# Kernel tuning notes

Measured on AMD Instinct MI355X. Metric: run time of the kernel, lower is better.

## Reference

```python
import jax, jax.numpy as jnp
import numpy as np

B, N, INP = 16, 1024, 256
HEADS, DIM_HEAD = 8, 32
INNER = HEADS * DIM_HEAD  # 256
OUP = 256
IH = IW = 32  # IH*IW == N


def _relative_index(ih, iw):
    # mirrors the torch __init__ construction (meshgrid indexing='ij')
    coords = np.stack(np.meshgrid(np.arange(ih), np.arange(iw), indexing='ij')).reshape(2, -1)
    rel = coords[:, :, None] - coords[:, None, :]  # [2, N, N]
    rel[0] += ih - 1
    rel[1] += iw - 1
    rel[0] *= 2 * iw - 1
    return rel.sum(0).reshape(-1)  # [N*N]


def setup_inputs() -> dict:
    key = jax.random.key(0)
    kx, kqkv, kout, kbias = jax.random.split(key, 4)
    x = jax.random.normal(kx, (B, N, INP), dtype=jnp.float32)
    w_qkv = jax.random.normal(kqkv, (INP, 3 * INNER), dtype=jnp.float32) * 0.02
    w_out = jax.random.normal(kout, (INNER, OUP), dtype=jnp.float32) * 0.02
    b_out = jnp.zeros((OUP,), dtype=jnp.float32)
    bias_table = jax.random.normal(kbias, ((2 * IH - 1) * (2 * IW - 1), HEADS), dtype=jnp.float32) * 0.02
    relative_index = jnp.asarray(_relative_index(IH, IW), dtype=jnp.int32)
    return {"x": x, "w_qkv": w_qkv, "w_out": w_out, "b_out": b_out,
            "bias_table": bias_table, "relative_index": relative_index}


def reference(x, w_qkv, w_out, b_out, bias_table, relative_index):
    b, n, _ = x.shape
    scale = DIM_HEAD ** (-0.5)
    qkv = x @ w_qkv  # [b, n, 3*inner]
    q, k, v = jnp.split(qkv, 3, axis=-1)
    split_heads = lambda t: t.reshape(b, n, HEADS, DIM_HEAD).transpose(0, 2, 1, 3)  # b h n d
    q, k, v = split_heads(q), split_heads(k), split_heads(v)
    dots = jnp.einsum('bhnd,bhmd->bhnm', q, k) * scale  # [b, h, n, n]
    # gather bias: (n*n, heads) -> (1, heads, n, n), matching '(h w) c -> 1 c h w'
    rel_bias = bias_table[relative_index].reshape(n, n, HEADS).transpose(2, 0, 1)[None]
    attn = jax.nn.softmax(dots + rel_bias, axis=-1)
    out = jnp.einsum('bhnm,bhmd->bhnd', attn, v)
    out = out.transpose(0, 2, 1, 3).reshape(b, n, INNER)  # b n (h d)
    return out @ w_out + b_out
```

## Files before the change

kernel.cpp:

```cpp
#include <hip/hip_runtime.h>
#include <hip/hip_bf16.h>

typedef __bf16 bf16;
typedef bf16 bf16x4 __attribute__((ext_vector_type(4)));
typedef bf16 bf16x8 __attribute__((ext_vector_type(8)));
typedef short s16x4 __attribute__((ext_vector_type(4)));
typedef float f32x4 __attribute__((ext_vector_type(4)));

#define MFMA32(A, B, C) __builtin_amdgcn_mfma_f32_16x16x32_bf16(A, B, C, 0, 0, 0)
#define MFMA16(A, B, C) __builtin_amdgcn_mfma_f32_16x16x16bf16_1k(A, B, C, 0, 0, 0)
#define GL2LDS16(gp, lp)                                                            \
  __builtin_amdgcn_global_load_lds((const __attribute__((address_space(1))) unsigned int*)(gp), \
                                   (__attribute__((address_space(3))) unsigned int*)(lp), 16, 0, 0)

static constexpr float SCALE = 0.17677669529663687f;
static constexpr float LOG2E = 1.4426950408889634f;

__global__ __launch_bounds__(256) void k_prep(const float* __restrict__ x,
                                              const float* __restrict__ wqkv,
                                              const float* __restrict__ wout,
                                              const float* __restrict__ table,
                                              const int* __restrict__ ridx,
                                              bf16* __restrict__ xb, bf16* __restrict__ wtq,
                                              bf16* __restrict__ wto, bf16* __restrict__ rbb) {
  const int tid = threadIdx.x;
  const int blk = blockIdx.x;
  if (blk < 2048) {
    int t = blk * 256 + tid;
    const float4* s = reinterpret_cast<const float4*>(x) + (size_t)t * 2;
    float4 a = s[0], c = s[1];
    bf16x8 o;
    o[0] = (bf16)a.x; o[1] = (bf16)a.y; o[2] = (bf16)a.z; o[3] = (bf16)a.w;
    o[4] = (bf16)c.x; o[5] = (bf16)c.y; o[6] = (bf16)c.z; o[7] = (bf16)c.w;
    reinterpret_cast<bf16x8*>(xb)[t] = o;
  } else if (blk < 3072) {
    int t = (blk - 2048) * 256 + tid;
    if (t < 196608) {
      int n = t >> 8, k = t & 255;
      wtq[t] = (bf16)wqkv[k * 768 + n];
    } else {
      int t2 = t - 196608;
      int n = t2 >> 8, k = t2 & 255;
      wto[t2] = (bf16)wout[k * 256 + n];
    }
  } else {
    const int bb2 = blk - 3072;
    const int qt = bb2 >> 6, kt = bb2 & 63;
    const int r = tid & 3, lane = tid >> 2;
    const int ln = lane & 15, quad = lane >> 4;
    const int qrow = qt * 16 + ln;
    const int key = kt * 16 + quad * 4 + r;
    const int idx = ridx[qrow * 1024 + key];
    const float4* p = reinterpret_cast<const float4*>(table) + idx * 2;
    float4 a = p[0], c = p[1];
    float vals[8] = {a.x, a.y, a.z, a.w, c.x, c.y, c.z, c.w};
    const int base = bb2 * 256 + tid;
#pragma unroll
    for (int h = 0; h < 8; ++h) rbb[h * 1048576 + base] = (bf16)(vals[h] * LOG2E);
  }
}

template <int EPI>
__global__ __launch_bounds__(256) void k_gemm(const bf16* __restrict__ A,
                                              const bf16* __restrict__ Bt,
                                              bf16* __restrict__ q, bf16* __restrict__ kk,
                                              bf16* __restrict__ vt, float* __restrict__ out,
                                              const float* __restrict__ bout) {
  __shared__ __align__(16) bf16 As[2][4096];
  __shared__ __align__(16) bf16 Bs[2][4096];
  const int tid = threadIdx.x;
  const int ln = tid & 15, quad = (tid >> 4) & 3, wv = tid >> 6;
  const int wm = (wv >> 1) * 64, wn = (wv & 1) * 64;
  const int m0 = blockIdx.x * 128, n0 = blockIdx.y * 128;
  const int srow = tid >> 2, scg = (tid & 3) * 8;
  const bf16* ag = A + (size_t)(m0 + srow) * 256 + scg;
  const bf16* bg = Bt + (size_t)(n0 + srow) * 256 + scg;
  f32x4 acc[4][4] = {};

  GL2LDS16(ag, &As[0][tid * 8]);
  GL2LDS16(ag + 64 * 256, &As[0][2048 + tid * 8]);
  GL2LDS16(bg, &Bs[0][tid * 8]);
  GL2LDS16(bg + 64 * 256, &Bs[0][2048 + tid * 8]);

#pragma unroll 2
  for (int kt = 0; kt < 256; kt += 32) {
    const int cur = (kt >> 5) & 1, nxt = cur ^ 1;
    __syncthreads();
    if (kt < 224) {
      GL2LDS16(ag + kt + 32, &As[nxt][tid * 8]);
      GL2LDS16(ag + 64 * 256 + kt + 32, &As[nxt][2048 + tid * 8]);
      GL2LDS16(bg + kt + 32, &Bs[nxt][tid * 8]);
      GL2LDS16(bg + 64 * 256 + kt + 32, &Bs[nxt][2048 + tid * 8]);
    }
    bf16x8 af[4], bfr[4];
#pragma unroll
    for (int i = 0; i < 4; ++i)
      af[i] = *reinterpret_cast<const bf16x8*>(&As[cur][(wm + i * 16 + ln) * 32 + quad * 8]);
#pragma unroll
    for (int i = 0; i < 4; ++i)
      bfr[i] = *reinterpret_cast<const bf16x8*>(&Bs[cur][(wn + i * 16 + ln) * 32 + quad * 8]);
#pragma unroll
    for (int i = 0; i < 4; ++i)
#pragma unroll
      for (int j = 0; j < 4; ++j) acc[i][j] = MFMA32(af[i], bfr[j], acc[i][j]);
  }

  if (EPI == 0) {
    const int colbase = n0 + wn;
    const int seg = colbase >> 8;
    const int cb = colbase & 255;
    const float mul = (seg == 0) ? SCALE * LOG2E : 1.0f;
#pragma unroll
    for (int i = 0; i < 4; ++i) {
      const int gm = m0 + wm + i * 16 + quad * 4;
      const int b = gm >> 10;
#pragma unroll
      for (int j = 0; j < 4; ++j) {
        const int gc = cb + j * 16 + ln;
        const int h = gc >> 5, d = gc & 31;
#pragma unroll
        for (int r = 0; r < 4; ++r) {
          const int nseq = (gm + r) & 1023;
          if (seg == 2) {
            vt[(b * 8 + h) * 32768 + d * 1024 + nseq] = (bf16)acc[i][j][r];
          } else {
            bf16* dst = (seg == 0) ? q : kk;
            dst[(b * 8 + h) * 32768 + nseq * 32 + d] = (bf16)(acc[i][j][r] * mul);
          }
        }
      }
    }
  } else {
#pragma unroll
    for (int j = 0; j < 4; ++j) {
      const int gc = n0 + wn + j * 16 + ln;
      const float bb = bout[gc];
#pragma unroll
      for (int i = 0; i < 4; ++i) {
        const int gm = m0 + wm + i * 16 + quad * 4;
#pragma unroll
        for (int r = 0; r < 4; ++r) out[(size_t)(gm + r) * 256 + gc] = acc[i][j][r] + bb;
      }
    }
  }
}

__global__ __launch_bounds__(256, 4) void k_flash(const bf16* __restrict__ qs,
                                                  const bf16* __restrict__ ks,
                                                  const bf16* __restrict__ vtg,
                                                  const bf16* __restrict__ rbb,
                                                  bf16* __restrict__ ao) {
  __shared__ __align__(16) bf16 Ks[2][2048];
  __shared__ __align__(16) bf16 Vs[2][2048];
  const int tid = threadIdx.x;
  const int lane = tid & 63;
  const int ln = lane & 15, quad = lane >> 4, wv = tid >> 6;
  const int blk = blockIdx.x;
  const int bh = blk & 127;
  const int b = bh >> 3, h = bh & 7;
  const int qtw = (blk >> 7) * 4 + wv;
  const int q0 = qtw * 32;
  const bf16* qb = qs + bh * 32768;
  const bf16* kb = ks + bh * 32768;
  const bf16* vb = vtg + bh * 32768;
  const bf16* bbias0 = rbb + h * 1048576 + (2 * qtw) * 16384 + lane * 4;
  const bf16* bbias1 = bbias0 + 16384;

  const bf16* kg = kb + (tid >> 2) * 32 + (((tid & 3) ^ ((tid >> 3) & 3)) * 8);
  const bf16* vg = vb + (tid >> 3) * 1024 + (((tid & 7) ^ ((tid >> 3) & 7)) * 8);

  const bf16x8 qfrag0 = *reinterpret_cast<const bf16x8*>(&qb[(q0 + ln) * 32 + quad * 8]);
  const bf16x8 qfrag1 = *reinterpret_cast<const bf16x8*>(&qb[(q0 + 16 + ln) * 32 + quad * 8]);

  const int ksw = (quad ^ ((ln >> 1) & 3)) * 8;
  const int vswl = ln & 7;

  f32x4 a00 = {0.f, 0.f, 0.f, 0.f}, a01 = {0.f, 0.f, 0.f, 0.f};
  f32x4 a10 = {0.f, 0.f, 0.f, 0.f}, a11 = {0.f, 0.f, 0.f, 0.f};
  float lsum0 = 0.f, lsum1 = 0.f;

  bf16x4 cbf[2][2][4];
#pragma unroll
  for (int nt = 0; nt < 4; ++nt) {
    cbf[0][0][nt] = *reinterpret_cast<const bf16x4*>(&bbias0[nt * 256]);
    cbf[0][1][nt] = *reinterpret_cast<const bf16x4*>(&bbias1[nt * 256]);
  }
  GL2LDS16(kg, &Ks[0][tid * 8]);
  GL2LDS16(vg, &Vs[0][tid * 8]);

#pragma unroll 2
  for (int it = 0; it < 16; ++it) {
    const int cur = it & 1, nxt = cur ^ 1;
    const int k0 = it * 64;
    __syncthreads();
    if (it < 15) {
      GL2LDS16(kg + (k0 + 64) * 32, &Ks[nxt][tid * 8]);
      GL2LDS16(vg + k0 + 64, &Vs[nxt][tid * 8]);
#pragma unroll
      for (int nt = 0; nt < 4; ++nt) {
        cbf[nxt][0][nt] = *reinterpret_cast<const bf16x4*>(&bbias0[((it + 1) * 4 + nt) * 256]);
        cbf[nxt][1][nt] = *reinterpret_cast<const bf16x4*>(&bbias1[((it + 1) * 4 + nt) * 256]);
      }
    }
    bf16x8 kf[4];
#pragma unroll
    for (int nt = 0; nt < 4; ++nt)
      kf[nt] = *reinterpret_cast<const bf16x8*>(&Ks[cur][(nt * 16 + ln) * 32 + ksw]);
    s16x4 vfa[4], vfc[4];
#pragma unroll
    for (int nt = 0; nt < 4; ++nt) {
      const int col = ((2 * nt + (quad >> 1)) ^ vswl) * 8 + (quad & 1) * 4;
      vfa[nt] = *reinterpret_cast<const s16x4*>(&Vs[cur][ln * 64 + col]);
      vfc[nt] = *reinterpret_cast<const s16x4*>(&Vs[cur][(ln + 16) * 64 + col]);
    }
    f32x4 s0[4], s1[4];
#pragma unroll
    for (int nt = 0; nt < 4; ++nt) {
      f32x4 c0, c1;
#pragma unroll
      for (int e = 0; e < 4; ++e) {
        c0[e] = (float)cbf[cur][0][nt][e];
        c1[e] = (float)cbf[cur][1][nt][e];
      }
      s0[nt] = MFMA32(kf[nt], qfrag0, c0);
      s1[nt] = MFMA32(kf[nt], qfrag1, c1);
    }
    s16x4 p0[4], p1[4];
#pragma unroll
    for (int nt = 0; nt < 4; ++nt) {
      bf16x4 t0, t1;
#pragma unroll
      for (int e = 0; e < 4; ++e) {
        s0[nt][e] = __builtin_amdgcn_exp2f(s0[nt][e]);
        t0[e] = (bf16)s0[nt][e];
        s1[nt][e] = __builtin_amdgcn_exp2f(s1[nt][e]);
        t1[e] = (bf16)s1[nt][e];
      }
      lsum0 += (s0[nt][0] + s0[nt][1]) + (s0[nt][2] + s0[nt][3]);
      lsum1 += (s1[nt][0] + s1[nt][1]) + (s1[nt][2] + s1[nt][3]);
      p0[nt] = __builtin_bit_cast(s16x4, t0);
      p1[nt] = __builtin_bit_cast(s16x4, t1);
    }
#pragma unroll
    for (int nt = 0; nt < 4; ++nt) {
      a00 = MFMA16(p0[nt], vfa[nt], a00);
      a01 = MFMA16(p0[nt], vfc[nt], a01);
      a10 = MFMA16(p1[nt], vfa[nt], a10);
      a11 = MFMA16(p1[nt], vfc[nt], a11);
    }
  }
  __syncthreads();

  lsum0 += __shfl_xor(lsum0, 16, 64);
  lsum0 += __shfl_xor(lsum0, 32, 64);
  lsum1 += __shfl_xor(lsum1, 16, 64);
  lsum1 += __shfl_xor(lsum1, 32, 64);

#pragma unroll
  for (int r = 0; r < 4; ++r) {
    const float inv0 = __builtin_amdgcn_rcpf(__shfl(lsum0, quad * 4 + r, 64));
    const int row0 = q0 + quad * 4 + r;
    bf16* po0 = &ao[(size_t)(b * 1024 + row0) * 256 + h * 32 + ln];
    po0[0] = (bf16)(a00[r] * inv0);
    po0[16] = (bf16)(a01[r] * inv0);
    const float inv1 = __builtin_amdgcn_rcpf(__shfl(lsum1, quad * 4 + r, 64));
    const int row1 = q0 + 16 + quad * 4 + r;
    bf16* po1 = &ao[(size_t)(b * 1024 + row1) * 256 + h * 32 + ln];
    po1[0] = (bf16)(a10[r] * inv1);
    po1[16] = (bf16)(a11[r] * inv1);
  }
}

extern "C" void kernel_launch(void* const* d_in, const int* in_sizes, int n_in,
                              void* d_out, int out_size, void* d_ws, size_t ws_size,
                              hipStream_t stream) {
  const float* x = (const float*)d_in[0];
  const float* wqkv = (const float*)d_in[1];
  const float* wout = (const float*)d_in[2];
  const float* bout = (const float*)d_in[3];
  const float* btab = (const float*)d_in[4];
  const int* ridx = (const int*)d_in[5];
  float* out = (float*)d_out;

  char* ws = (char*)d_ws;
  bf16* xb  = (bf16*)(ws + 0);
  bf16* wtq = (bf16*)(ws + 8388608);
  bf16* wto = (bf16*)(ws + 8781824);
  bf16* q   = (bf16*)(ws + 8912896);
  bf16* k   = (bf16*)(ws + 17301504);
  bf16* vt  = (bf16*)(ws + 25690112);
  bf16* rb  = (bf16*)(ws + 34078720);
  bf16* ao  = (bf16*)(ws + 50855936);

  k_prep<<<7168, 256, 0, stream>>>(x, wqkv, wout, btab, ridx, xb, wtq, wto, rb);
  k_gemm<0><<<dim3(128, 6), 256, 0, stream>>>(xb, wtq, q, k, vt, nullptr, nullptr);
  k_flash<<<1024, 256, 0, stream>>>(q, k, vt, rb, ao);
  k_gemm<1><<<dim3(128, 2), 256, 0, stream>>>(ao, wto, nullptr, nullptr, nullptr, out, bout);
}
```

Measured before the change: 150.1 us.

## Triple-buffer K/V LDS tiles with explicit vmcnt waits in flash kernel

Moves the flash attention K/V staging from double to triple buffering, prefetching two tiles ahead. A single s_barrier is gated on a partial vmcnt wait instead of the full __syncthreads drain. Scheduling barriers pin the order of prefetches and bias loads, and s_setprio raises wave priority around the MFMA blocks. This aims to hide global-to-LDS latency better, at the cost of more LDS per block (possibly lower occupancy) and a hand-counted vmcnt that must match the number of outstanding loads. Redundant clamped prefetches on the last iterations add a little extra traffic.

```diff
diff --git a/kernel.cpp b/kernel.cpp
--- a/kernel.cpp
+++ b/kernel.cpp
@@ -12,6 +12,7 @@
 #define GL2LDS16(gp, lp)                                                            \
   __builtin_amdgcn_global_load_lds((const __attribute__((address_space(1))) unsigned int*)(gp), \
                                    (__attribute__((address_space(3))) unsigned int*)(lp), 16, 0, 0)
+#define SCHEDB() __builtin_amdgcn_sched_barrier(0)
 
 static constexpr float SCALE = 0.17677669529663687f;
 static constexpr float LOG2E = 1.4426950408889634f;
@@ -150,8 +151,8 @@
                                                   const bf16* __restrict__ vtg,
                                                   const bf16* __restrict__ rbb,
                                                   bf16* __restrict__ ao) {
-  __shared__ __align__(16) bf16 Ks[2][2048];
-  __shared__ __align__(16) bf16 Vs[2][2048];
+  __shared__ __align__(16) bf16 Ks[3][2048];
+  __shared__ __align__(16) bf16 Vs[3][2048];
   const int tid = threadIdx.x;
   const int lane = tid & 63;
   const int ln = lane & 15, quad = lane >> 4, wv = tid >> 6;
@@ -169,9 +170,6 @@
   const bf16* kg = kb + (tid >> 2) * 32 + (((tid & 3) ^ ((tid >> 3) & 3)) * 8);
   const bf16* vg = vb + (tid >> 3) * 1024 + (((tid & 7) ^ ((tid >> 3) & 7)) * 8);
 
-  const bf16x8 qfrag0 = *reinterpret_cast<const bf16x8*>(&qb[(q0 + ln) * 32 + quad * 8]);
-  const bf16x8 qfrag1 = *reinterpret_cast<const bf16x8*>(&qb[(q0 + 16 + ln) * 32 + quad * 8]);
-
   const int ksw = (quad ^ ((ln >> 1) & 3)) * 8;
   const int vswl = ln & 7;
 
@@ -179,29 +177,45 @@
   f32x4 a10 = {0.f, 0.f, 0.f, 0.f}, a11 = {0.f, 0.f, 0.f, 0.f};
   float lsum0 = 0.f, lsum1 = 0.f;
 
+  GL2LDS16(kg, &Ks[0][tid * 8]);
+  GL2LDS16(vg, &Vs[0][tid * 8]);
+  GL2LDS16(kg + 2048, &Ks[1][tid * 8]);
+  GL2LDS16(vg + 64, &Vs[1][tid * 8]);
+  SCHEDB();
   bf16x4 cbf[2][2][4];
 #pragma unroll
   for (int nt = 0; nt < 4; ++nt) {
     cbf[0][0][nt] = *reinterpret_cast<const bf16x4*>(&bbias0[nt * 256]);
     cbf[0][1][nt] = *reinterpret_cast<const bf16x4*>(&bbias1[nt * 256]);
   }
-  GL2LDS16(kg, &Ks[0][tid * 8]);
-  GL2LDS16(vg, &Vs[0][tid * 8]);
+  const bf16x8 qfrag0 = *reinterpret_cast<const bf16x8*>(&qb[(q0 + ln) * 32 + quad * 8]);
+  const bf16x8 qfrag1 = *reinterpret_cast<const bf16x8*>(&qb[(q0 + 16 + ln) * 32 + quad * 8]);
+  SCHEDB();
 
 #pragma unroll 2
   for (int it = 0; it < 16; ++it) {
-    const int cur = it & 1, nxt = cur ^ 1;
-    const int k0 = it * 64;
-    __syncthreads();
-    if (it < 15) {
-      GL2LDS16(kg + (k0 + 64) * 32, &Ks[nxt][tid * 8]);
-      GL2LDS16(vg + k0 + 64, &Vs[nxt][tid * 8]);
+    const int cur = it % 3;
+    const int pre = (it + 2) % 3;
+    const int cb_cur = it & 1, cb_nxt = cb_cur ^ 1;
+    asm volatile("s_waitcnt vmcnt(8)" ::: "memory");
+    SCHEDB();
+    __builtin_amdgcn_s_barrier();
+    SCHEDB();
+    {
+      const int pf = (it + 2 <= 15) ? (it + 2) : 15;
+      GL2LDS16(kg + pf * 2048, &Ks[pre][tid * 8]);
+      GL2LDS16(vg + pf * 64, &Vs[pre][tid * 8]);
+    }
+    SCHEDB();
+    {
+      const int bn = (it + 1 <= 15) ? (it + 1) : 15;
 #pragma unroll
       for (int nt = 0; nt < 4; ++nt) {
-        cbf[nxt][0][nt] = *reinterpret_cast<const bf16x4*>(&bbias0[((it + 1) * 4 + nt) * 256]);
-        cbf[nxt][1][nt] = *reinterpret_cast<const bf16x4*>(&bbias1[((it + 1) * 4 + nt) * 256]);
-      }
-    }
+        cbf[cb_nxt][0][nt] = *reinterpret_cast<const bf16x4*>(&bbias0[(bn * 4 + nt) * 256]);
+        cbf[cb_nxt][1][nt] = *reinterpret_cast<const bf16x4*>(&bbias1[(bn * 4 + nt) * 256]);
+      }
+    }
+    SCHEDB();
     bf16x8 kf[4];
 #pragma unroll
     for (int nt = 0; nt < 4; ++nt)
@@ -214,17 +228,19 @@
       vfc[nt] = *reinterpret_cast<const s16x4*>(&Vs[cur][(ln + 16) * 64 + col]);
     }
     f32x4 s0[4], s1[4];
+    __builtin_amdgcn_s_setprio(1);
 #pragma unroll
     for (int nt = 0; nt < 4; ++nt) {
       f32x4 c0, c1;
 #pragma unroll
       for (int e = 0; e < 4; ++e) {
-        c0[e] = (float)cbf[cur][0][nt][e];
-        c1[e] = (float)cbf[cur][1][nt][e];
+        c0[e] = (float)cbf[cb_cur][0][nt][e];
+        c1[e] = (float)cbf[cb_cur][1][nt][e];
       }
       s0[nt] = MFMA32(kf[nt], qfrag0, c0);
       s1[nt] = MFMA32(kf[nt], qfrag1, c1);
     }
+    __builtin_amdgcn_s_setprio(0);
     s16x4 p0[4], p1[4];
 #pragma unroll
     for (int nt = 0; nt < 4; ++nt) {
@@ -241,6 +257,7 @@
       p0[nt] = __builtin_bit_cast(s16x4, t0);
       p1[nt] = __builtin_bit_cast(s16x4, t1);
     }
+    __builtin_amdgcn_s_setprio(1);
 #pragma unroll
     for (int nt = 0; nt < 4; ++nt) {
       a00 = MFMA16(p0[nt], vfa[nt], a00);
@@ -248,6 +265,7 @@
       a10 = MFMA16(p1[nt], vfa[nt], a10);
       a11 = MFMA16(p1[nt], vfc[nt], a11);
     }
+    __builtin_amdgcn_s_setprio(0);
   }
   __syncthreads();
 
```

After: 151.3 us. No clear change (+0.8%).
